# Optimization experiments

Measured on AMD Instinct MI355X. Metric: run time of the kernel, lower is better.

## Reference

```python
import jax, jax.numpy as jnp
import numpy as np
from jax import lax

B, D, H, W = 1, 8, 64, 64
C, WS, NH = 192, 8, 6
N = WS ** 3          # 512 tokens per window
HD = C // NH         # 32
CONV_SCALE = 0.01
EPS = 1e-5
DN = ('NCDHW', 'OIDHW', 'NCDHW')


def _make_rpi():
    c = np.stack(np.meshgrid(np.arange(WS), np.arange(WS), np.arange(WS), indexing='ij')).reshape(3, -1)
    rel = (c[:, :, None] - c[:, None, :]).transpose(1, 2, 0) + (WS - 1)  # [N,N,3]
    idx = rel[..., 0] * (2 * WS - 1) ** 2 + rel[..., 1] * (2 * WS - 1) + rel[..., 2]
    return jnp.asarray(idx, dtype=jnp.int32)


def _ln(x, g, b):
    m = x.mean(-1, keepdims=True)
    v = jnp.mean((x - m) ** 2, -1, keepdims=True)
    return (x - m) * lax.rsqrt(v + EPS) * g + b


def setup_inputs() -> dict:
    key = jax.random.key(0)
    ks = jax.random.split(key, 16)
    s = 0.02
    inp = {
        'x': jax.random.normal(ks[0], (B, D * H * W, C), jnp.float32),
        'norm1_g': jnp.ones((C,), jnp.float32), 'norm1_b': jnp.zeros((C,), jnp.float32),
        'qkv_w': jax.random.normal(ks[1], (3 * C, C), jnp.float32) * s,
        'qkv_b': jnp.zeros((3 * C,), jnp.float32),
        'rpb_table': jax.random.normal(ks[2], (3375, NH), jnp.float32) * s,
        'proj_w': jax.random.normal(ks[3], (C, C), jnp.float32) * s,
        'proj_b': jnp.zeros((C,), jnp.float32),
        'conv1_w': jax.random.normal(ks[4], (C // 3, C, 3, 3, 3), jnp.float32) * s,
        'conv1_b': jnp.zeros((C // 3,), jnp.float32),
        'conv2_w': jax.random.normal(ks[5], (C, C // 3, 3, 3, 3), jnp.float32) * s,
        'conv2_b': jnp.zeros((C,), jnp.float32),
        'ca1_w': jax.random.normal(ks[6], (6, C), jnp.float32) * s,
        'ca1_b': jnp.zeros((6,), jnp.float32),
        'ca2_w': jax.random.normal(ks[7], (C, 6), jnp.float32) * s,
        'ca2_b': jnp.zeros((C,), jnp.float32),
        'norm2_g': jnp.ones((C,), jnp.float32), 'norm2_b': jnp.zeros((C,), jnp.float32),
        'fc1_w': jax.random.normal(ks[8], (4 * C, C), jnp.float32) * s,
        'fc1_b': jnp.zeros((4 * C,), jnp.float32),
        'fc2_w': jax.random.normal(ks[9], (C, 4 * C), jnp.float32) * s,
        'fc2_b': jnp.zeros((C,), jnp.float32),
        'rpi': _make_rpi(),
    }
    return inp


def reference(x, norm1_g, norm1_b, qkv_w, qkv_b, rpb_table, proj_w, proj_b,
              conv1_w, conv1_b, conv2_w, conv2_b, ca1_w, ca1_b, ca2_w, ca2_b,
              norm2_g, norm2_b, fc1_w, fc1_b, fc2_w, fc2_b, rpi):
    shortcut = x
    xn = _ln(x, norm1_g, norm1_b)                      # [B, L, C]
    x5 = xn.reshape(B, D, H, W, C)

    # ---- CAB3D conv branch (conv3x3 -> gelu -> conv3x3 -> channel attention)
    xc = jnp.transpose(x5, (0, 4, 1, 2, 3))            # NCDHW
    h = lax.conv_general_dilated(xc, conv1_w, (1, 1, 1), 'SAME', dimension_numbers=DN)
    h = jax.nn.gelu(h + conv1_b[None, :, None, None, None], approximate=False)
    h = lax.conv_general_dilated(h, conv2_w, (1, 1, 1), 'SAME', dimension_numbers=DN)
    h = h + conv2_b[None, :, None, None, None]
    pooled = h.mean(axis=(2, 3, 4))                    # [B, C] global avg pool
    a = jax.nn.relu(pooled @ ca1_w.T + ca1_b)
    a = jax.nn.sigmoid(a @ ca2_w.T + ca2_b)            # [B, C]
    conv_x = (h * a[:, :, None, None, None])
    conv_x = jnp.transpose(conv_x, (0, 2, 3, 4, 1)).reshape(B, D * H * W, C)

    # ---- window partition (shift_size forced to 0 since min(res)==window_size)
    xw = x5.reshape(B, D // WS, WS, H // WS, WS, W // WS, WS, C)
    xw = jnp.transpose(xw, (0, 1, 3, 5, 2, 4, 6, 7)).reshape(-1, N, C)  # [nW, N, C]

    # ---- window attention with relative position bias
    qkv = (xw @ qkv_w.T + qkv_b).reshape(-1, N, 3, NH, HD)
    q = jnp.transpose(qkv[:, :, 0], (0, 2, 1, 3)) * (HD ** -0.5)  # [nW, h, N, d]
    k = jnp.transpose(qkv[:, :, 1], (0, 2, 1, 3))
    v = jnp.transpose(qkv[:, :, 2], (0, 2, 1, 3))
    attn = jnp.einsum('whnd,whmd->whnm', q, k)
    bias = rpb_table[rpi]                              # [N, N, h]
    attn = attn + jnp.transpose(bias, (2, 0, 1))[None]
    attn = jax.nn.softmax(attn, axis=-1)
    out = jnp.einsum('whnm,whmd->whnd', attn, v)
    out = jnp.transpose(out, (0, 2, 1, 3)).reshape(-1, N, C)
    out = out @ proj_w.T + proj_b

    # ---- window reverse
    out = out.reshape(B, D // WS, H // WS, W // WS, WS, WS, WS, C)
    out = jnp.transpose(out, (0, 1, 4, 2, 5, 3, 6, 7)).reshape(B, D * H * W, C)

    x2 = shortcut + out + conv_x * CONV_SCALE
    xm = _ln(x2, norm2_g, norm2_b)
    xm = jax.nn.gelu(xm @ fc1_w.T + fc1_b, approximate=False) @ fc2_w.T + fc2_b
    return x2 + xm
```

## Files before the change

### kernel.cpp

```cpp
#include <hip/hip_runtime.h>
#include <hip/hip_bf16.h>

#define LTOK  32768
#define CDIM  192
#define DD_   8
#define HH_   64
#define WW_   64
#define NHEAD 6
#define HDIM  32
#define NWIN  64
#define NTOKW 512
#define C3    64
#define FCH   768

#define OFF_XN     0u
#define OFF_QH     6291456u
#define OFF_KH     9437184u
#define OFF_VH     12582912u
#define OFF_Y      15728640u
#define OFF_YBF    18874368u
#define OFF_H1     22020096u
#define OFF_H2     24117248u
#define OFF_PART   30408704u
#define OFF_AMASK  30457856u
#define OFF_BIAST  30458048u
#define OFF_W1T    32030912u
#define OFF_W2T    32362688u
#define OFF_QKVT   32694464u
#define OFF_PROJT  32805056u
#define OFF_FC1T   32841920u
#define OFF_FC2T   32989376u

typedef __attribute__((ext_vector_type(8)))  short short8v;
typedef __attribute__((ext_vector_type(16))) float f32x16;

union FragU { short8v v; unsigned u[4]; };

__device__ __forceinline__ float gelu_exact(float x) {
    return 0.5f * x * (1.0f + erff(x * 0.70710678118654752f));
}

__device__ __forceinline__ unsigned short bf16bits(float x) {
    union { __hip_bfloat16 b; unsigned short u; } cv;
    cv.b = __float2bfloat16(x);
    return cv.u;
}

__global__ __launch_bounds__(256) void k_ln(const float* __restrict__ in,
                                            const float* __restrict__ g,
                                            const float* __restrict__ b,
                                            float* __restrict__ out,
                                            __hip_bfloat16* __restrict__ obf) {
    int wv = threadIdx.x >> 6, lane = threadIdx.x & 63;
    int t = blockIdx.x * 4 + wv;
    const float* row = in + (size_t)t * CDIM;
    float x0 = row[lane], x1 = row[lane + 64], x2 = row[lane + 128];
    float s = x0 + x1 + x2;
    for (int o = 32; o; o >>= 1) s += __shfl_xor(s, o);
    float m = s * (1.0f / 192.0f);
    float d0 = x0 - m, d1 = x1 - m, d2 = x2 - m;
    float vv = d0 * d0 + d1 * d1 + d2 * d2;
    for (int o = 32; o; o >>= 1) vv += __shfl_xor(vv, o);
    float inv = rsqrtf(vv * (1.0f / 192.0f) + 1e-5f);
    size_t base = (size_t)t * CDIM;
    float y0 = d0 * inv * g[lane]       + b[lane];
    float y1 = d1 * inv * g[lane + 64]  + b[lane + 64];
    float y2 = d2 * inv * g[lane + 128] + b[lane + 128];
    if (out) {
        out[base + lane]       = y0;
        out[base + lane + 64]  = y1;
        out[base + lane + 128] = y2;
    }
    if (obf) {
        obf[base + lane]       = __float2bfloat16(y0);
        obf[base + lane + 64]  = __float2bfloat16(y1);
        obf[base + lane + 128] = __float2bfloat16(y2);
    }
}

__global__ void k_wpack(const float* __restrict__ w, __hip_bfloat16* __restrict__ wp,
                        int R, int C) {
    int i = blockIdx.x * 256 + threadIdx.x;
    if (i >= R * C) return;
    int j = i & 7, l31 = (i >> 3) & 31, half = (i >> 8) & 1;
    int rest = i >> 9;
    int nkc = C >> 4;
    int kc = rest % nkc, rt = rest / nkc;
    int row = rt * 32 + l31, col = kc * 16 + half * 8 + j;
    wp[i] = __float2bfloat16(w[(size_t)row * C + col]);
}

__global__ void k_wp1(const float* __restrict__ w, __hip_bfloat16* __restrict__ wp) {
    int i = blockIdx.x * 256 + threadIdx.x;
    if (i >= 331776) return;
    int j = i & 7, oc = (i >> 3) & 63, h = (i >> 9) & 1;
    int cg = (i >> 10) % 12, kk = i / 12288;
    int c = cg * 16 + h * 8 + j;
    wp[i] = __float2bfloat16(w[((size_t)oc * 192 + c) * 27 + kk]);
}
__global__ void k_wp2(const float* __restrict__ w, __hip_bfloat16* __restrict__ wp) {
    int i = blockIdx.x * 256 + threadIdx.x;
    if (i >= 331776) return;
    int j = i & 7, oc = (i >> 3) % 192;
    int h = (i / 1536) & 1, cg = (i / 3072) & 3, kk = i / 12288;
    int c = cg * 16 + h * 8 + j;
    wp[i] = __float2bfloat16(w[((size_t)oc * 64 + c) * 27 + kk]);
}

__global__ __launch_bounds__(256) void k_bias(const int* __restrict__ rpi,
                                              const float* __restrict__ rpb,
                                              float* __restrict__ biasT) {
    __shared__ int idxl[64][64];
    int tid = threadIdx.x;
    int n0 = (blockIdx.x >> 3) * 64, m0 = (blockIdx.x & 7) * 64;
    for (int it = 0; it < 16; it++) {
        int e = it * 256 + tid;
        int ln_ = e >> 6, lm = e & 63;
        idxl[ln_][lm] = rpi[(size_t)(n0 + ln_) * NTOKW + m0 + lm];
    }
    __syncthreads();
    for (int it = 0; it < 16; it++) {
        int e = it * 256 + tid;
        int lm = e >> 6, ln_ = e & 63;
        int id = idxl[ln_][lm];
        #pragma unroll
        for (int h = 0; h < NHEAD; h++)
            biasT[(size_t)h * NTOKW * NTOKW + (size_t)(m0 + lm) * NTOKW + n0 + ln_] =
                rpb[id * NHEAD + h];
    }
}

__global__ __launch_bounds__(256) void k_conv1m(const __hip_bfloat16* __restrict__ xnbf,
                                                const __hip_bfloat16* __restrict__ w1p,
                                                const float* __restrict__ b1,
                                                __hip_bfloat16* __restrict__ h1bf) {
    __shared__ __align__(16) char lds[66 * 384];
    int tid = threadIdx.x;
    int wv = tid >> 6, lane = tid & 63;
    int wr = wv >> 1, wc = wv & 1;
    int half = lane >> 5, l31 = lane & 31;
    int row = blockIdx.x;
    int d = row >> 6, hh = row & 63;

    if (tid < 48) {
        float4 z = {0.f, 0.f, 0.f, 0.f};
        char* p = lds + ((tid < 24) ? tid * 16 : 65 * 384 + (tid - 24) * 16);
        *(float4*)p = z;
    }

    f32x16 acc;
    #pragma unroll
    for (int r = 0; r < 16; r++) acc[r] = 0.f;

    for (int kd = -1; kd <= 1; kd++) {
        int dd = d + kd;
        if (dd < 0 || dd >= DD_) continue;
        for (int kh = -1; kh <= 1; kh++) {
            int h2 = hh + kh;
            if (h2 < 0 || h2 >= HH_) continue;
            const short* src = (const short*)xnbf + ((size_t)((dd << 12) | (h2 << 6))) * CDIM;
            __syncthreads();
            #pragma unroll
            for (int it = 0; it < 6; it++) {
                int e16 = it * 256 + tid;
                int tok = e16 / 24, cb = (e16 % 24) * 16;
                short8v vdat = *(const short8v*)(src + e16 * 8);
                int lrow = tok + 1;
                *(short8v*)(lds + lrow * 384 + (cb ^ ((lrow & 7) << 4))) = vdat;
            }
            __syncthreads();
            #pragma unroll
            for (int kw = -1; kw <= 1; kw++) {
                int kk = (kd + 1) * 9 + (kh + 1) * 3 + (kw + 1);
                int atok = 32 * wr + l31 + kw + 1;
                int akey = (atok & 7) << 4;
                const char* abase = lds + atok * 384;
                const short* wbase = (const short*)w1p + (kk * 24 + half) * 512 + (32 * wc + l31) * 8;
                #pragma unroll
                for (int cg = 0; cg < 12; cg++) {
                    short8v af = *(const short8v*)(abase + ((cg * 32 + half * 16) ^ akey));
                    short8v bf = *(const short8v*)(wbase + cg * 1024);
                    acc = __builtin_amdgcn_mfma_f32_32x32x16_bf16(af, bf, acc, 0, 0, 0);
                }
            }
        }
    }
    int oc = 32 * wc + l31;
    float bb = b1[oc];
    int t0 = row * 64;
    #pragma unroll
    for (int r = 0; r < 16; r++) {
        int tok = 32 * wr + (r & 3) + 8 * (r >> 2) + 4 * half;
        h1bf[(size_t)(t0 + tok) * C3 + oc] = __float2bfloat16(gelu_exact(acc[r] + bb));
    }
}

__global__ __launch_bounds__(384) void k_conv2m(const __hip_bfloat16* __restrict__ h1bf,
                                                const __hip_bfloat16* __restrict__ w2p,
                                                const float* __restrict__ b2,
                                                float* __restrict__ h2) {
    __shared__ __align__(16) char lds[34 * 128];
    int tid = threadIdx.x;
    int wv = tid >> 6, lane = tid & 63;
    int half = lane >> 5, l31 = lane & 31;
    int row = blockIdx.x >> 1, hr = blockIdx.x & 1;
    int d = row >> 6, hh = row & 63;

    f32x16 acc;
    #pragma unroll
    for (int r = 0; r < 16; r++) acc[r] = 0.f;

    for (int kd = -1; kd <= 1; kd++) {
        int dd = d + kd;
        if (dd < 0 || dd >= DD_) continue;
        for (int kh = -1; kh <= 1; kh++) {
            int h2r = hh + kh;
            if (h2r < 0 || h2r >= HH_) continue;
            __syncthreads();
            if (tid < 272) {
                int ti = tid >> 3, cb = (tid & 7) * 16;
                int w = hr * 32 + ti - 1;
                short8v vdat = {0, 0, 0, 0, 0, 0, 0, 0};
                if (w >= 0 && w < 64)
                    vdat = *(const short8v*)((const short*)h1bf +
                           (size_t)((dd << 12) | (h2r << 6) | w) * C3 + cb / 2);
                *(short8v*)(lds + ti * 128 + (cb ^ ((ti & 7) << 4))) = vdat;
            }
            __syncthreads();
            #pragma unroll
            for (int kw = -1; kw <= 1; kw++) {
                int kk = (kd + 1) * 9 + (kh + 1) * 3 + (kw + 1);
                int atok = l31 + kw + 1;
                int akey = (atok & 7) << 4;
                const char* abase = lds + atok * 128;
                const short* wbase = (const short*)w2p + (kk * 8 + half) * 1536 + (wv * 32 + l31) * 8;
                #pragma unroll
                for (int cg = 0; cg < 4; cg++) {
                    short8v af = *(const short8v*)(abase + ((cg * 32 + half * 16) ^ akey));
                    short8v bf = *(const short8v*)(wbase + cg * 3072);
                    acc = __builtin_amdgcn_mfma_f32_32x32x16_bf16(af, bf, acc, 0, 0, 0);
                }
            }
        }
    }
    int oc = wv * 32 + l31;
    float bb = b2[oc];
    int t0 = row * 64 + hr * 32;
    #pragma unroll
    for (int r = 0; r < 16; r++) {
        int tok = (r & 3) + 8 * (r >> 2) + 4 * half;
        h2[(size_t)(t0 + tok) * CDIM + oc] = acc[r] + bb;
    }
}

__global__ __launch_bounds__(192) void k_pool(const float* __restrict__ h2,
                                              float* __restrict__ part) {
    int c = threadIdx.x, b = blockIdx.x;
    float s = 0.f;
    for (int i = 0; i < 128; i++) s += h2[(size_t)(b * 128 + i) * CDIM + c];
    part[b * CDIM + c] = s;
}

__global__ __launch_bounds__(192) void k_ca(const float* __restrict__ part,
                                            const float* __restrict__ ca1w,
                                            const float* __restrict__ ca1b,
                                            const float* __restrict__ ca2w,
                                            const float* __restrict__ ca2b,
                                            float* __restrict__ amask) {
    __shared__ float pooled[CDIM];
    __shared__ float hid[6];
    int c = threadIdx.x;
    float s = 0.f;
    for (int b = 0; b < 256; b++) s += part[b * CDIM + c];
    pooled[c] = s * (1.0f / 32768.0f);
    __syncthreads();
    if (c < 6) {
        float a = ca1b[c];
        for (int j = 0; j < CDIM; j++) a += ca1w[c * CDIM + j] * pooled[j];
        hid[c] = fmaxf(a, 0.f);
    }
    __syncthreads();
    float a = ca2b[c];
    for (int j = 0; j < 6; j++) a += ca2w[c * 6 + j] * hid[j];
    amask[c] = 1.0f / (1.0f + expf(-a));
}

__global__ __launch_bounds__(192) void k_qkvm(const __hip_bfloat16* __restrict__ xnbf,
                                              const __hip_bfloat16* __restrict__ qwb,
                                              const float* __restrict__ qkvb,
                                              __hip_bfloat16* __restrict__ q,
                                              __hip_bfloat16* __restrict__ k,
                                              __hip_bfloat16* __restrict__ v) {
    __shared__ __align__(16) char xlds[32 * 384];
    __shared__ float tb[3][32][33];
    int tid = threadIdx.x;
    int wv = tid >> 6, lane = tid & 63;
    int half = lane >> 5, l31 = lane & 31;
    int t0 = blockIdx.x * 32;
    int wi = t0 >> 9;
    int wh_ = wi >> 3, ww_ = wi & 7;

    #pragma unroll
    for (int it = 0; it < 4; it++) {
        int e16 = it * 192 + tid;
        int tok = e16 / 24, cb = (e16 % 24) * 16;
        int n = (t0 + tok) & 511;
        int nd = n >> 6, nh = (n >> 3) & 7, nw = n & 7;
        int torig = (nd << 12) | ((wh_ * 8 + nh) << 6) | (ww_ * 8 + nw);
        short8v vdat = *(const short8v*)((const short*)xnbf + (size_t)torig * CDIM + (e16 % 24) * 8);
        *(short8v*)(xlds + tok * 384 + (cb ^ ((tok & 7) << 4))) = vdat;
    }
    __syncthreads();

    int akey = (l31 & 7) << 4;
    const char* xbase = xlds + l31 * 384;
    __hip_bfloat16* dstbase = (wv == 0) ? q : (wv == 1 ? k : v);
    float scale = (wv == 0) ? 0.17677669529663687f : 1.0f;

    for (int j = 0; j < 6; j++) {
        int ti = wv * 6 + j;
        f32x16 a0, a1;
        #pragma unroll
        for (int r = 0; r < 16; r++) { a0[r] = 0.f; a1[r] = 0.f; }
        const short* wbase = (const short*)qwb + ti * 6144 + half * 256 + l31 * 8;
        #pragma unroll
        for (int cg = 0; cg < 12; cg += 2) {
            short8v bf0 = *(const short8v*)(xbase + ((cg * 32 + half * 16) ^ akey));
            short8v bf1 = *(const short8v*)(xbase + (((cg + 1) * 32 + half * 16) ^ akey));
            short8v af0 = *(const short8v*)(wbase + cg * 512);
            short8v af1 = *(const short8v*)(wbase + (cg + 1) * 512);
            a0 = __builtin_amdgcn_mfma_f32_32x32x16_bf16(af0, bf0, a0, 0, 0, 0);
            a1 = __builtin_amdgcn_mfma_f32_32x32x16_bf16(af1, bf1, a1, 0, 0, 0);
        }
        #pragma unroll
        for (int r = 0; r < 16; r++) {
            int dl = (r & 3) + 8 * (r >> 2) + 4 * half;
            tb[wv][l31][dl] = a0[r] + a1[r];
        }
        asm volatile("s_waitcnt lgkmcnt(0)" ::: "memory");
        __builtin_amdgcn_sched_barrier(0);
        int tok = lane >> 1, d0 = (lane & 1) * 16;
        int n = (t0 + tok) & 511;
        __hip_bfloat16* dst = dstbase +
                              ((size_t)((wi * NHEAD + j) * NTOKW + n)) * HDIM + d0;
        const float* bp = qkvb + ti * 32 + d0;
        short8v o0, o1;
        #pragma unroll
        for (int i = 0; i < 8; i++)
            o0[i] = (short)bf16bits((tb[wv][tok][d0 + i] + bp[i]) * scale);
        #pragma unroll
        for (int i = 0; i < 8; i++)
            o1[i] = (short)bf16bits((tb[wv][tok][d0 + 8 + i] + bp[8 + i]) * scale);
        *(short8v*)((short*)dst) = o0;
        *(short8v*)((short*)dst + 8) = o1;
        asm volatile("s_waitcnt lgkmcnt(0)" ::: "memory");
        __builtin_amdgcn_sched_barrier(0);
    }
}

__global__ __launch_bounds__(256) void k_attn(const __hip_bfloat16* __restrict__ qh,
                                              const __hip_bfloat16* __restrict__ kh,
                                              const __hip_bfloat16* __restrict__ vh,
                                              const float* __restrict__ biasT,
                                              __hip_bfloat16* __restrict__ outbf) {
    __shared__ float ot[4][32][33];
    int wv = threadIdx.x >> 6, lane = threadIdx.x & 63;
    int tile = blockIdx.x * 4 + wv;
    int qt = tile & 15, wh = tile >> 4;
    int head = wh % NHEAD, wi = wh / NHEAD;
    int qb = qt * 32;
    int h = lane >> 5, ln31 = lane & 31;

    const unsigned short* qp = (const unsigned short*)qh + ((size_t)wh * NTOKW + qb + ln31) * HDIM;
    short8v qf0 = *(const short8v*)(qp + 8 * h);
    short8v qf1 = *(const short8v*)(qp + 16 + 8 * h);
    const unsigned short* kbase = (const unsigned short*)kh + (size_t)wh * NTOKW * HDIM;
    const unsigned short* vbase = (const unsigned short*)vh + (size_t)wh * NTOKW * HDIM;
    const float* bbase = biasT + (size_t)head * NTOKW * NTOKW + qb + ln31;

    f32x16 O;
    #pragma unroll
    for (int r = 0; r < 16; r++) O[r] = 0.f;
    float m = -1e30f, l = 0.f;

    for (int kb = 0; kb < NTOKW; kb += 32) {
        const unsigned short* kp = kbase + (size_t)(kb + ln31) * HDIM;
        short8v kf0 = *(const short8v*)(kp + 8 * h);
        short8v kf1 = *(const short8v*)(kp + 16 + 8 * h);
        f32x16 S;
        #pragma unroll
        for (int r = 0; r < 16; r++) S[r] = 0.f;
        S = __builtin_amdgcn_mfma_f32_32x32x16_bf16(kf0, qf0, S, 0, 0, 0);
        S = __builtin_amdgcn_mfma_f32_32x32x16_bf16(kf1, qf1, S, 0, 0, 0);

        float s[16];
        #pragma unroll
        for (int r = 0; r < 16; r++) {
            int key = (r & 3) + 8 * (r >> 2) + 4 * h;
            s[r] = S[r] + bbase[(size_t)(kb + key) * NTOKW];
        }
        float cm = s[0];
        #pragma unroll
        for (int r = 1; r < 16; r++) cm = fmaxf(cm, s[r]);
        cm = fmaxf(cm, __shfl_xor(cm, 32));
        float mn = fmaxf(m, cm);
        float scale = __expf(m - mn);
        float e[16]; float cs = 0.f;
        #pragma unroll
        for (int r = 0; r < 16; r++) { e[r] = __expf(s[r] - mn); cs += e[r]; }
        cs += __shfl_xor(cs, 32);
        l = l * scale + cs;
        m = mn;
        #pragma unroll
        for (int r = 0; r < 16; r++) O[r] *= scale;

        unsigned P[8], Qx[8];
        #pragma unroll
        for (int i = 0; i < 8; i++)
            P[i] = (unsigned)bf16bits(e[2 * i]) | ((unsigned)bf16bits(e[2 * i + 1]) << 16);
        #pragma unroll
        for (int i = 0; i < 8; i++) Qx[i] = __shfl_xor(P[i], 32);

        FragU p0, p1;
        p0.u[0] = h ? Qx[2] : P[0];  p0.u[1] = h ? Qx[3] : P[1];
        p0.u[2] = h ? P[2]  : Qx[0]; p0.u[3] = h ? P[3]  : Qx[1];
        p1.u[0] = h ? Qx[6] : P[4];  p1.u[1] = h ? Qx[7] : P[5];
        p1.u[2] = h ? P[6]  : Qx[4]; p1.u[3] = h ? P[7]  : Qx[5];

        const unsigned short* vp0 = vbase + (size_t)(kb + 8 * h) * HDIM + ln31;
        const unsigned short* vp1 = vbase + (size_t)(kb + 16 + 8 * h) * HDIM + ln31;
        short8v vf0, vf1;
        #pragma unroll
        for (int i = 0; i < 8; i++) {
            vf0[i] = (short)vp0[i * HDIM];
            vf1[i] = (short)vp1[i * HDIM];
        }
        O = __builtin_amdgcn_mfma_f32_32x32x16_bf16(vf0, p0.v, O, 0, 0, 0);
        O = __builtin_amdgcn_mfma_f32_32x32x16_bf16(vf1, p1.v, O, 0, 0, 0);
    }

    float invl = 1.0f / l;
    #pragma unroll
    for (int r = 0; r < 16; r++) {
        int d = (r & 3) + 8 * (r >> 2) + 4 * h;
        ot[wv][ln31][d] = O[r] * invl;
    }
    __syncthreads();
    int t2 = lane >> 1, c0 = (lane & 1) * 16;
    short* outp = (short*)outbf + ((size_t)(wi * NTOKW + qb + t2)) * CDIM + head * HDIM + c0;
    short8v s0, s1;
    #pragma unroll
    for (int i = 0; i < 8; i++) s0[i] = (short)bf16bits(ot[wv][t2][c0 + i]);
    #pragma unroll
    for (int i = 0; i < 8; i++) s1[i] = (short)bf16bits(ot[wv][t2][c0 + 8 + i]);
    *(short8v*)outp = s0;
    *(short8v*)(outp + 8) = s1;
}

__global__ __launch_bounds__(192) void k_projm(const __hip_bfloat16* __restrict__ attnbf,
                                               const __hip_bfloat16* __restrict__ pwb,
                                               const float* __restrict__ pb,
                                               const float* __restrict__ x,
                                               const float* __restrict__ h2,
                                               const float* __restrict__ amask,
                                               float* __restrict__ x2) {
    __shared__ __align__(16) char alds[32 * 384];
    __shared__ float tb[3][32][33];
    int tid = threadIdx.x;
    int wv = tid >> 6, lane = tid & 63;
    int half = lane >> 5, l31 = lane & 31;
    int t0 = blockIdx.x * 32;
    int wi = t0 >> 9;
    int wh_ = wi >> 3, ww_ = wi & 7;

    const short* src = (const short*)attnbf + (size_t)t0 * CDIM;
    #pragma unroll
    for (int it = 0; it < 4; it++) {
        int e16 = it * 192 + tid;
        int tok = e16 / 24, cb = (e16 % 24) * 16;
        short8v vdat = *(const short8v*)(src + e16 * 8);
        *(short8v*)(alds + tok * 384 + (cb ^ ((tok & 7) << 4))) = vdat;
    }
    __syncthreads();

    int akey = (l31 & 7) << 4;
    const char* abase = alds + l31 * 384;

    for (int j = 0; j < 2; j++) {
        int ot = wv * 2 + j;
        f32x16 a0, a1;
        #pragma unroll
        for (int r = 0; r < 16; r++) { a0[r] = 0.f; a1[r] = 0.f; }
        const short* wbase = (const short*)pwb + ot * 6144 + half * 256 + l31 * 8;
        #pragma unroll
        for (int cg = 0; cg < 12; cg += 2) {
            short8v bf0 = *(const short8v*)(abase + ((cg * 32 + half * 16) ^ akey));
            short8v bf1 = *(const short8v*)(abase + (((cg + 1) * 32 + half * 16) ^ akey));
            short8v af0 = *(const short8v*)(wbase + cg * 512);
            short8v af1 = *(const short8v*)(wbase + (cg + 1) * 512);
            a0 = __builtin_amdgcn_mfma_f32_32x32x16_bf16(af0, bf0, a0, 0, 0, 0);
            a1 = __builtin_amdgcn_mfma_f32_32x32x16_bf16(af1, bf1, a1, 0, 0, 0);
        }
        #pragma unroll
        for (int r = 0; r < 16; r++) {
            int oc = (r & 3) + 8 * (r >> 2) + 4 * half;
            tb[wv][l31][oc] = a0[r] + a1[r];
        }
        asm volatile("s_waitcnt lgkmcnt(0)" ::: "memory");
        __builtin_amdgcn_sched_barrier(0);
        int tok = lane >> 1, c0 = (lane & 1) * 16;
        int n = (t0 + tok) & 511;
        int nd = n >> 6, nh = (n >> 3) & 7, nw = n & 7;
        int t = (nd << 12) | ((wh_ * 8 + nh) << 6) | (ww_ * 8 + nw);
        size_t idx = (size_t)t * CDIM + ot * 32 + c0;
        const float* bp = pb + ot * 32 + c0;
        const float* ap = amask + ot * 32 + c0;
        #pragma unroll
        for (int i = 0; i < 16; i++)
            x2[idx + i] = x[idx + i] + tb[wv][tok][c0 + i] + bp[i] + 0.01f * h2[idx + i] * ap[i];
        asm volatile("s_waitcnt lgkmcnt(0)" ::: "memory");
        __builtin_amdgcn_sched_barrier(0);
    }
}

__global__ __launch_bounds__(256) void k_mlpm(const __hip_bfloat16* __restrict__ ybf,
                                              const __hip_bfloat16* __restrict__ w1b,
                                              const float* __restrict__ b1,
                                              const __hip_bfloat16* __restrict__ w2b,
                                              const float* __restrict__ b2,
                                              float* __restrict__ out) {
    __shared__ __align__(16) char ylds[32 * 384];
    __shared__ __align__(16) float rbuf[6 * 32 * 32];
    int tid = threadIdx.x;
    int wv = tid >> 6, lane = tid & 63;
    int half = lane >> 5, l31 = lane & 31;
    int t0 = blockIdx.x * 32;

    const short* src = (const short*)ybf + (size_t)t0 * CDIM;
    #pragma unroll
    for (int it = 0; it < 3; it++) {
        int e16 = it * 256 + tid;
        int tok = e16 / 24, cb = (e16 % 24) * 16;
        short8v vdat = *(const short8v*)(src + e16 * 8);
        *(short8v*)(ylds + tok * 384 + (cb ^ ((tok & 7) << 4))) = vdat;
    }
    __syncthreads();

    int akey = (l31 & 7) << 4;
    const char* ybase = ylds + l31 * 384;

    f32x16 oacc[6];
    #pragma unroll
    for (int ot = 0; ot < 6; ot++)
        #pragma unroll
        for (int r = 0; r < 16; r++) oacc[ot][r] = 0.f;

    for (int j = 0; j < 6; j++) {
        int hc = wv * 6 + j;
        f32x16 h0, h1;
        #pragma unroll
        for (int r = 0; r < 16; r++) { h0[r] = 0.f; h1[r] = 0.f; }
        const short* w1base = (const short*)w1b + hc * 6144 + half * 256 + l31 * 8;
        #pragma unroll
        for (int cg = 0; cg < 12; cg += 2) {
            short8v bf0 = *(const short8v*)(ybase + ((cg * 32 + half * 16) ^ akey));
            short8v bf1 = *(const short8v*)(ybase + (((cg + 1) * 32 + half * 16) ^ akey));
            short8v af0 = *(const short8v*)(w1base + cg * 512);
            short8v af1 = *(const short8v*)(w1base + (cg + 1) * 512);
            h0 = __builtin_amdgcn_mfma_f32_32x32x16_bf16(af0, bf0, h0, 0, 0, 0);
            h1 = __builtin_amdgcn_mfma_f32_32x32x16_bf16(af1, bf1, h1, 0, 0, 0);
        }
        float e[16];
        #pragma unroll
        for (int r = 0; r < 16; r++) {
            int hid = (r & 3) + 8 * (r >> 2) + 4 * half;
            e[r] = gelu_exact(h0[r] + h1[r] + b1[hc * 32 + hid]);
        }
        unsigned P[8], Qx[8];
        #pragma unroll
        for (int i = 0; i < 8; i++)
            P[i] = (unsigned)bf16bits(e[2 * i]) | ((unsigned)bf16bits(e[2 * i + 1]) << 16);
        #pragma unroll
        for (int i = 0; i < 8; i++) Qx[i] = __shfl_xor(P[i], 32);
        FragU p0, p1;
        p0.u[0] = half ? Qx[2] : P[0];  p0.u[1] = half ? Qx[3] : P[1];
        p0.u[2] = half ? P[2]  : Qx[0]; p0.u[3] = half ? P[3]  : Qx[1];
        p1.u[0] = half ? Qx[6] : P[4];  p1.u[1] = half ? Qx[7] : P[5];
        p1.u[2] = half ? P[6]  : Qx[4]; p1.u[3] = half ? P[7]  : Qx[5];

        const short* w2base = (const short*)w2b + hc * 1024 + half * 256 + l31 * 8;
        #pragma unroll
        for (int ot = 0; ot < 6; ot++) {
            short8v a0 = *(const short8v*)(w2base + ot * 24576);
            short8v a1 = *(const short8v*)(w2base + ot * 24576 + 512);
            oacc[ot] = __builtin_amdgcn_mfma_f32_32x32x16_bf16(a0, p0.v, oacc[ot], 0, 0, 0);
            oacc[ot] = __builtin_amdgcn_mfma_f32_32x32x16_bf16(a1, p1.v, oacc[ot], 0, 0, 0);
        }
    }

    float4* rb4 = (float4*)rbuf;
    for (int w = 0; w < 4; w++) {
        if (wv == w) {
            #pragma unroll
            for (int ot = 0; ot < 6; ot++) {
                #pragma unroll
                for (int g = 0; g < 4; g++) {
                    float4 val = {oacc[ot][g * 4 + 0], oacc[ot][g * 4 + 1],
                                  oacc[ot][g * 4 + 2], oacc[ot][g * 4 + 3]};
                    int chunk = 2 * g + half;
                    float4* p = &rb4[(ot * 32 + l31) * 8 + (chunk ^ (l31 & 7))];
                    if (w == 0) *p = val;
                    else {
                        float4 o = *p;
                        o.x += val.x; o.y += val.y; o.z += val.z; o.w += val.w;
                        *p = o;
                    }
                }
            }
        }
        __syncthreads();
    }

    #pragma unroll
    for (int i = 0; i < 6; i++) {
        int c4 = i * 256 + tid;
        int oc4 = c4 & 7;
        int tok = (c4 >> 3) & 31;
        int ot  = c4 >> 8;
        float4 vv = rb4[(ot * 32 + tok) * 8 + (oc4 ^ (tok & 7))];
        float* op = out + (size_t)(t0 + tok) * CDIM + ot * 32 + oc4 * 4;
        const float* bp = b2 + ot * 32 + oc4 * 4;
        op[0] += vv.x + bp[0];
        op[1] += vv.y + bp[1];
        op[2] += vv.z + bp[2];
        op[3] += vv.w + bp[3];
    }
}

extern "C" void kernel_launch(void* const* d_in, const int* in_sizes, int n_in,
                              void* d_out, int out_size, void* d_ws, size_t ws_size,
                              hipStream_t stream) {
    const float* x     = (const float*)d_in[0];
    const float* n1g   = (const float*)d_in[1];
    const float* n1b   = (const float*)d_in[2];
    const float* qkvw  = (const float*)d_in[3];
    const float* qkvb  = (const float*)d_in[4];
    const float* rpb   = (const float*)d_in[5];
    const float* projw = (const float*)d_in[6];
    const float* projb = (const float*)d_in[7];
    const float* c1w   = (const float*)d_in[8];
    const float* c1b   = (const float*)d_in[9];
    const float* c2w   = (const float*)d_in[10];
    const float* c2b   = (const float*)d_in[11];
    const float* ca1w  = (const float*)d_in[12];
    const float* ca1b  = (const float*)d_in[13];
    const float* ca2w  = (const float*)d_in[14];
    const float* ca2b  = (const float*)d_in[15];
    const float* n2g   = (const float*)d_in[16];
    const float* n2b   = (const float*)d_in[17];
    const float* fc1w  = (const float*)d_in[18];
    const float* fc1b  = (const float*)d_in[19];
    const float* fc2w  = (const float*)d_in[20];
    const float* fc2b  = (const float*)d_in[21];
    const int*   rpi   = (const int*)d_in[22];

    float* ws  = (float*)d_ws;
    float* out = (float*)d_out;

    __hip_bfloat16* attnbf = (__hip_bfloat16*)(ws + OFF_XN);
    __hip_bfloat16* qh   = (__hip_bfloat16*)(ws + OFF_QH);
    __hip_bfloat16* kb_  = (__hip_bfloat16*)(ws + OFF_KH);
    __hip_bfloat16* vb_  = (__hip_bfloat16*)(ws + OFF_VH);
    __hip_bfloat16* xnbf = (__hip_bfloat16*)(ws + OFF_Y);
    __hip_bfloat16* ybf  = (__hip_bfloat16*)(ws + OFF_YBF);
    __hip_bfloat16* h1bf = (__hip_bfloat16*)(ws + OFF_H1);
    float* h2    = ws + OFF_H2;
    float* part  = ws + OFF_PART;
    float* amask = ws + OFF_AMASK;
    float* biasT = ws + OFF_BIAST;
    __hip_bfloat16* w1p  = (__hip_bfloat16*)(ws + OFF_W1T);
    __hip_bfloat16* w2p  = (__hip_bfloat16*)(ws + OFF_W2T);
    __hip_bfloat16* qwb  = (__hip_bfloat16*)(ws + OFF_QKVT);
    __hip_bfloat16* pwb  = (__hip_bfloat16*)(ws + OFF_PROJT);
    __hip_bfloat16* w1b  = (__hip_bfloat16*)(ws + OFF_FC1T);
    __hip_bfloat16* w2b  = (__hip_bfloat16*)(ws + OFF_FC2T);

    k_wp1<<<(331776 + 255) / 256, 256, 0, stream>>>(c1w, w1p);
    k_wp2<<<(331776 + 255) / 256, 256, 0, stream>>>(c2w, w2p);
    k_wpack<<<(110592 + 255) / 256, 256, 0, stream>>>(qkvw, qwb, 576, 192);
    k_wpack<<<(36864 + 255) / 256, 256, 0, stream>>>(projw, pwb, 192, 192);
    k_wpack<<<(147456 + 255) / 256, 256, 0, stream>>>(fc1w, w1b, 768, 192);
    k_wpack<<<(147456 + 255) / 256, 256, 0, stream>>>(fc2w, w2b, 192, 768);
    k_bias<<<64, 256, 0, stream>>>(rpi, rpb, biasT);

    k_ln<<<LTOK / 4, 256, 0, stream>>>(x, n1g, n1b, (float*)nullptr, xnbf);
    k_conv1m<<<512, 256, 0, stream>>>(xnbf, w1p, c1b, h1bf);
    k_conv2m<<<1024, 384, 0, stream>>>(h1bf, w2p, c2b, h2);
    k_pool<<<256, 192, 0, stream>>>(h2, part);
    k_ca<<<1, 192, 0, stream>>>(part, ca1w, ca1b, ca2w, ca2b, amask);
    k_qkvm<<<LTOK / 32, 192, 0, stream>>>(xnbf, qwb, qkvb, qh, kb_, vb_);
    k_attn<<<(NWIN * NHEAD * 16) / 4, 256, 0, stream>>>(qh, kb_, vb_, biasT, attnbf);
    k_projm<<<LTOK / 32, 192, 0, stream>>>(attnbf, pwb, projb, x, h2, amask, out);
    k_ln<<<LTOK / 4, 256, 0, stream>>>(out, n2g, n2b, (float*)nullptr, ybf);
    k_mlpm<<<LTOK / 32, 256, 0, stream>>>(ybf, w1b, fc1b, w2b, fc2b, out);
}
```

Measured before the change: 384.3 us.

## Fuse LayerNorm2 into projection epilogue, merge weight packing, use tanh GELU

```diff
diff --git a/kernel.cpp b/kernel.cpp
--- a/kernel.cpp
+++ b/kernel.cpp
@@ -36,8 +36,11 @@
 
 union FragU { short8v v; unsigned u[4]; };
 
-__device__ __forceinline__ float gelu_exact(float x) {
-    return 0.5f * x * (1.0f + erff(x * 0.70710678118654752f));
+__device__ __forceinline__ float gelu_fast(float x) {
+    float z = 0.7978845608028654f * (x + 0.044715f * x * x * x);
+    float e = __expf(2.0f * z);
+    float t = 1.0f - 2.0f / (e + 1.0f);
+    return 0.5f * x * (1.0f + t);
 }
 
 __device__ __forceinline__ unsigned short bf16bits(float x) {
@@ -78,10 +81,9 @@
     }
 }
 
-__global__ void k_wpack(const float* __restrict__ w, __hip_bfloat16* __restrict__ wp,
-                        int R, int C) {
-    int i = blockIdx.x * 256 + threadIdx.x;
-    if (i >= R * C) return;
+__device__ __forceinline__ void wpack_one(const float* __restrict__ w,
+                                          __hip_bfloat16* __restrict__ wp,
+                                          int i, int C) {
     int j = i & 7, l31 = (i >> 3) & 31, half = (i >> 8) & 1;
     int rest = i >> 9;
     int nkc = C >> 4;
@@ -90,21 +92,33 @@
     wp[i] = __float2bfloat16(w[(size_t)row * C + col]);
 }
 
-__global__ void k_wp1(const float* __restrict__ w, __hip_bfloat16* __restrict__ wp) {
+__global__ void k_prep(const float* __restrict__ c1w, const float* __restrict__ c2w,
+                       const float* __restrict__ qkvw, const float* __restrict__ projw,
+                       const float* __restrict__ fc1w, const float* __restrict__ fc2w,
+                       __hip_bfloat16* __restrict__ w1p, __hip_bfloat16* __restrict__ w2p,
+                       __hip_bfloat16* __restrict__ qwb, __hip_bfloat16* __restrict__ pwb,
+                       __hip_bfloat16* __restrict__ w1b, __hip_bfloat16* __restrict__ w2b) {
     int i = blockIdx.x * 256 + threadIdx.x;
-    if (i >= 331776) return;
-    int j = i & 7, oc = (i >> 3) & 63, h = (i >> 9) & 1;
-    int cg = (i >> 10) % 12, kk = i / 12288;
-    int c = cg * 16 + h * 8 + j;
-    wp[i] = __float2bfloat16(w[((size_t)oc * 192 + c) * 27 + kk]);
-}
-__global__ void k_wp2(const float* __restrict__ w, __hip_bfloat16* __restrict__ wp) {
-    int i = blockIdx.x * 256 + threadIdx.x;
-    if (i >= 331776) return;
-    int j = i & 7, oc = (i >> 3) % 192;
-    int h = (i / 1536) & 1, cg = (i / 3072) & 3, kk = i / 12288;
-    int c = cg * 16 + h * 8 + j;
-    wp[i] = __float2bfloat16(w[((size_t)oc * 64 + c) * 27 + kk]);
+    if (i < 331776) {
+        int j = i & 7, oc = (i >> 3) & 63, h = (i >> 9) & 1;
+        int cg = (i >> 10) % 12, kk = i / 12288;
+        int c = cg * 16 + h * 8 + j;
+        w1p[i] = __float2bfloat16(c1w[((size_t)oc * 192 + c) * 27 + kk]);
+    } else if (i < 663552) {
+        int t = i - 331776;
+        int j = t & 7, oc = (t >> 3) % 192;
+        int h = (t / 1536) & 1, cg = (t / 3072) & 3, kk = t / 12288;
+        int c = cg * 16 + h * 8 + j;
+        w2p[t] = __float2bfloat16(c2w[((size_t)oc * 64 + c) * 27 + kk]);
+    } else if (i < 774144) {
+        wpack_one(qkvw, qwb, i - 663552, 192);
+    } else if (i < 811008) {
+        wpack_one(projw, pwb, i - 774144, 192);
+    } else if (i < 958464) {
+        wpack_one(fc1w, w1b, i - 811008, 192);
+    } else if (i < 1105920) {
+        wpack_one(fc2w, w2b, i - 958464, 768);
+    }
 }
 
 __global__ __launch_bounds__(256) void k_bias(const int* __restrict__ rpi,
@@ -191,7 +205,7 @@
     #pragma unroll
     for (int r = 0; r < 16; r++) {
         int tok = 32 * wr + (r & 3) + 8 * (r >> 2) + 4 * half;
-        h1bf[(size_t)(t0 + tok) * C3 + oc] = __float2bfloat16(gelu_exact(acc[r] + bb));
+        h1bf[(size_t)(t0 + tok) * C3 + oc] = __float2bfloat16(gelu_fast(acc[r] + bb));
     }
 }
 
@@ -463,9 +477,12 @@
                                                const float* __restrict__ x,
                                                const float* __restrict__ h2,
                                                const float* __restrict__ amask,
-                                               float* __restrict__ x2) {
+                                               const float* __restrict__ n2g,
+                                               const float* __restrict__ n2b,
+                                               float* __restrict__ x2,
+                                               __hip_bfloat16* __restrict__ ybf) {
     __shared__ __align__(16) char alds[32 * 384];
-    __shared__ float tb[3][32][33];
+    __shared__ float xls[32][193];
     int tid = threadIdx.x;
     int wv = tid >> 6, lane = tid & 63;
     int half = lane >> 5, l31 = lane & 31;
@@ -504,22 +521,48 @@
         #pragma unroll
         for (int r = 0; r < 16; r++) {
             int oc = (r & 3) + 8 * (r >> 2) + 4 * half;
-            tb[wv][l31][oc] = a0[r] + a1[r];
-        }
-        asm volatile("s_waitcnt lgkmcnt(0)" ::: "memory");
-        __builtin_amdgcn_sched_barrier(0);
-        int tok = lane >> 1, c0 = (lane & 1) * 16;
+            xls[l31][ot * 32 + oc] = a0[r] + a1[r];
+        }
+    }
+    __syncthreads();
+
+    #pragma unroll
+    for (int it = 0; it < 8; it++) {
+        int c4 = it * 192 + tid;
+        int tok = c4 / 48, cc = (c4 % 48) * 4;
         int n = (t0 + tok) & 511;
         int nd = n >> 6, nh = (n >> 3) & 7, nw = n & 7;
         int t = (nd << 12) | ((wh_ * 8 + nh) << 6) | (ww_ * 8 + nw);
-        size_t idx = (size_t)t * CDIM + ot * 32 + c0;
-        const float* bp = pb + ot * 32 + c0;
-        const float* ap = amask + ot * 32 + c0;
-        #pragma unroll
-        for (int i = 0; i < 16; i++)
-            x2[idx + i] = x[idx + i] + tb[wv][tok][c0 + i] + bp[i] + 0.01f * h2[idx + i] * ap[i];
-        asm volatile("s_waitcnt lgkmcnt(0)" ::: "memory");
-        __builtin_amdgcn_sched_barrier(0);
+        size_t idx = (size_t)t * CDIM + cc;
+        float4 xv = *(const float4*)(x + idx);
+        float4 hv = *(const float4*)(h2 + idx);
+        float v0 = xv.x + xls[tok][cc + 0] + pb[cc + 0] + 0.01f * hv.x * amask[cc + 0];
+        float v1 = xv.y + xls[tok][cc + 1] + pb[cc + 1] + 0.01f * hv.y * amask[cc + 1];
+        float v2 = xv.z + xls[tok][cc + 2] + pb[cc + 2] + 0.01f * hv.z * amask[cc + 2];
+        float v3 = xv.w + xls[tok][cc + 3] + pb[cc + 3] + 0.01f * hv.w * amask[cc + 3];
+        float4 ov = {v0, v1, v2, v3};
+        *(float4*)(x2 + idx) = ov;
+        xls[tok][cc + 0] = v0; xls[tok][cc + 1] = v1;
+        xls[tok][cc + 2] = v2; xls[tok][cc + 3] = v3;
+    }
+    __syncthreads();
+
+    for (int tok = wv; tok < 32; tok += 3) {
+        float v0 = xls[tok][lane], v1 = xls[tok][lane + 64], v2 = xls[tok][lane + 128];
+        float s = v0 + v1 + v2;
+        for (int o = 32; o; o >>= 1) s += __shfl_xor(s, o);
+        float mean = s * (1.0f / 192.0f);
+        float d0 = v0 - mean, d1 = v1 - mean, d2 = v2 - mean;
+        float vv = d0 * d0 + d1 * d1 + d2 * d2;
+        for (int o = 32; o; o >>= 1) vv += __shfl_xor(vv, o);
+        float inv = rsqrtf(vv * (1.0f / 192.0f) + 1e-5f);
+        int n = (t0 + tok) & 511;
+        int nd = n >> 6, nh = (n >> 3) & 7, nw = n & 7;
+        int t = (nd << 12) | ((wh_ * 8 + nh) << 6) | (ww_ * 8 + nw);
+        size_t base = (size_t)t * CDIM;
+        ybf[base + lane]       = __float2bfloat16(d0 * inv * n2g[lane]       + n2b[lane]);
+        ybf[base + lane + 64]  = __float2bfloat16(d1 * inv * n2g[lane + 64]  + n2b[lane + 64]);
+        ybf[base + lane + 128] = __float2bfloat16(d2 * inv * n2g[lane + 128] + n2b[lane + 128]);
     }
 }
 
@@ -574,7 +617,7 @@
         #pragma unroll
         for (int r = 0; r < 16; r++) {
             int hid = (r & 3) + 8 * (r >> 2) + 4 * half;
-            e[r] = gelu_exact(h0[r] + h1[r] + b1[hc * 32 + hid]);
+            e[r] = gelu_fast(h0[r] + h1[r] + b1[hc * 32 + hid]);
         }
         unsigned P[8], Qx[8];
         #pragma unroll
@@ -685,12 +728,8 @@
     __hip_bfloat16* w1b  = (__hip_bfloat16*)(ws + OFF_FC1T);
     __hip_bfloat16* w2b  = (__hip_bfloat16*)(ws + OFF_FC2T);
 
-    k_wp1<<<(331776 + 255) / 256, 256, 0, stream>>>(c1w, w1p);
-    k_wp2<<<(331776 + 255) / 256, 256, 0, stream>>>(c2w, w2p);
-    k_wpack<<<(110592 + 255) / 256, 256, 0, stream>>>(qkvw, qwb, 576, 192);
-    k_wpack<<<(36864 + 255) / 256, 256, 0, stream>>>(projw, pwb, 192, 192);
-    k_wpack<<<(147456 + 255) / 256, 256, 0, stream>>>(fc1w, w1b, 768, 192);
-    k_wpack<<<(147456 + 255) / 256, 256, 0, stream>>>(fc2w, w2b, 192, 768);
+    k_prep<<<(1105920 + 255) / 256, 256, 0, stream>>>(c1w, c2w, qkvw, projw, fc1w, fc2w,
+                                                      w1p, w2p, qwb, pwb, w1b, w2b);
     k_bias<<<64, 256, 0, stream>>>(rpi, rpb, biasT);
 
     k_ln<<<LTOK / 4, 256, 0, stream>>>(x, n1g, n1b, (float*)nullptr, xnbf);
@@ -700,7 +739,6 @@
     k_ca<<<1, 192, 0, stream>>>(part, ca1w, ca1b, ca2w, ca2b, amask);
     k_qkvm<<<LTOK / 32, 192, 0, stream>>>(xnbf, qwb, qkvb, qh, kb_, vb_);
     k_attn<<<(NWIN * NHEAD * 16) / 4, 256, 0, stream>>>(qh, kb_, vb_, biasT, attnbf);
-    k_projm<<<LTOK / 32, 192, 0, stream>>>(attnbf, pwb, projb, x, h2, amask, out);
-    k_ln<<<LTOK / 4, 256, 0, stream>>>(out, n2g, n2b, (float*)nullptr, ybf);
+    k_projm<<<LTOK / 32, 192, 0, stream>>>(attnbf, pwb, projb, x, h2, amask, n2g, n2b, out, ybf);
     k_mlpm<<<LTOK / 32, 256, 0, stream>>>(ybf, w1b, fc1b, w2b, fc2b, out);
 }
```

Result: no change. 382.9 us (-0.4%).
